# Performance work log

Measured on AMD Instinct MI355X. Metric: run time of the kernel, lower is better.

The kernel has to match this reference:

```python
import jax, jax.numpy as jnp
import numpy as np

L, H, NH, I = 6, 768, 12, 3072
DH = H // NH
EPS = 1e-12


def setup_inputs() -> dict:
    key = jax.random.key(0)
    ks = jax.random.split(key, 17)
    B, S = 16, 512
    s = lambda k, shape, fan: jax.random.normal(k, shape, jnp.float32) * (1.0 / np.sqrt(fan))
    return {
        "hidden_states": jax.random.normal(ks[0], (B, S, H), jnp.float32),
        "Wq": s(ks[1], (L, H, H), H), "bq": jnp.zeros((L, H), jnp.float32),
        "Wk": s(ks[2], (L, H, H), H), "bk": jnp.zeros((L, H), jnp.float32),
        "Wv": s(ks[3], (L, H, H), H), "bv": jnp.zeros((L, H), jnp.float32),
        "Wo": s(ks[4], (L, H, H), H), "bo": jnp.zeros((L, H), jnp.float32),
        "g1": jnp.ones((L, H), jnp.float32), "b1": jnp.zeros((L, H), jnp.float32),
        "Wi": s(ks[5], (L, H, I), H), "bi": jnp.zeros((L, I), jnp.float32),
        "Wo2": s(ks[6], (L, I, H), I), "bo2": jnp.zeros((L, H), jnp.float32),
        "g2": jnp.ones((L, H), jnp.float32), "b2": jnp.zeros((L, H), jnp.float32),
    }


def _layernorm(x, g, b):
    m = jnp.mean(x, axis=-1, keepdims=True)
    v = jnp.mean(jnp.square(x - m), axis=-1, keepdims=True)
    return (x - m) * jax.lax.rsqrt(v + EPS) * g + b


def _encoder(h, params):
    def layer_fn(h, p):
        Wq, bq, Wk, bk, Wv, bv, Wo, bo, g1, b1, Wi, bi, Wo2, bo2, g2, b2 = p
        B, S, _ = h.shape
        q = (h @ Wq + bq).reshape(B, S, NH, DH)
        k = (h @ Wk + bk).reshape(B, S, NH, DH)
        v = (h @ Wv + bv).reshape(B, S, NH, DH)
        scores = jnp.einsum("bshd,bthd->bhst", q, k) / np.sqrt(DH).astype(np.float32)
        probs = jax.nn.softmax(scores, axis=-1)  # dropout is identity in eval
        ctx = jnp.einsum("bhst,bthd->bshd", probs, v).reshape(B, S, H)
        attn_out = _layernorm(ctx @ Wo + bo + h, g1, b1)
        inter = jax.nn.gelu(attn_out @ Wi + bi, approximate=False)
        out = _layernorm(inter @ Wo2 + bo2 + attn_out, g2, b2)
        return out, None

    h, _ = jax.lax.scan(layer_fn, h, params)
    return h


def reference(hidden_states, Wq, bq, Wk, bk, Wv, bv, Wo, bo, g1, b1, Wi, bi, Wo2, bo2, g2, b2):
    params = (Wq, bq, Wk, bk, Wv, bv, Wo, bo, g1, b1, Wi, bi, Wo2, bo2, g2, b2)
    return _encoder(hidden_states, params)
```

## Files before the change

### kernel.cpp

```cpp
#include <hip/hip_runtime.h>
#include <hip/hip_bf16.h>
#include <math.h>

#define LNUM  6
#define HDIM  768
#define NHEAD 12
#define DHEAD 64
#define IDIM  3072
#define NB    16
#define SEQ   512
#define MTOK  (NB*SEQ)
#define NQKV  (3*HDIM)

typedef __bf16 bf16;
typedef __bf16 bf16x4 __attribute__((ext_vector_type(4)));
typedef __bf16 bf16x8 __attribute__((ext_vector_type(8)));
typedef float  f32x4  __attribute__((ext_vector_type(4)));

__device__ __forceinline__ void async_copy16(const bf16* g, bf16* l) {
  __builtin_amdgcn_global_load_lds((__attribute__((address_space(1))) void*)g,
                                   (__attribute__((address_space(3))) void*)l,
                                   16, 0, 0);
}

__device__ __forceinline__ float gelu_fast(float t) {
  const float u = 0.7978845608f * (t + 0.044715f * t * t * t);
  const float e = __expf(-2.f * fabsf(u));
  const float th = (1.f - e) / (1.f + e);
  return 0.5f * t * (1.f + copysignf(th, u));
}

__global__ void detect_k(const unsigned short* __restrict__ probe, int* __restrict__ flag)
{
  __shared__ int sc[4];
  const int tid = threadIdx.x;
  int cnt = 0;
#pragma unroll
  for (int j = 0; j < 16; j++) {
    const unsigned short w = probe[tid * 16 + j];
    const int e = (w >> 7) & 0xFF;
    cnt += (e >= 90 && e <= 130) ? 1 : 0;
  }
#pragma unroll
  for (int o = 32; o; o >>= 1) cnt += __shfl_xor(cnt, o);
  if ((tid & 63) == 0) sc[tid >> 6] = cnt;
  __syncthreads();
  if (tid == 0) flag[0] = ((sc[0] + sc[1] + sc[2] + sc[3]) < 3482) ? 1 : 0;
}

__global__ void cvt1d_k(const void* __restrict__ src, bf16* __restrict__ dst,
                        int n, const int* __restrict__ flag)
{
  const int i = blockIdx.x * 256 + threadIdx.x;
  if (i < n)
    dst[i] = (*flag) ? (bf16)((const float*)src)[i] : ((const bf16*)src)[i];
}

__global__ void cvt_slice_k(const void* __restrict__ src, bf16* __restrict__ dst,
                            int perL, int off, int dstStride, int total,
                            const int* __restrict__ flag)
{
  const int i = blockIdx.x * 256 + threadIdx.x;
  if (i < total) {
    const int l = i / perL, c = i - l * perL;
    const bf16 v = (*flag) ? (bf16)((const float*)src)[i] : ((const bf16*)src)[i];
    dst[l * dstStride + off + c] = v;
  }
}

__global__ void wtrans_k(const void* __restrict__ src, bf16* __restrict__ dst,
                         int K, int N, int layer, int dstLS, int dstOff,
                         const int* __restrict__ flag)
{
  __shared__ bf16 t[32][33];
  const size_t sOff = (size_t)(blockIdx.z + layer) * K * N;
  const size_t dOff = (size_t)blockIdx.z * dstLS + dstOff;
  const int n0 = blockIdx.x * 32, k0 = blockIdx.y * 32;
  const int tx = threadIdx.x, ty = threadIdx.y;
  const int f = *flag;
#pragma unroll
  for (int i = 0; i < 4; i++) {
    const size_t idx = sOff + (size_t)(k0 + ty*4 + i) * N + n0 + tx;
    t[ty*4+i][tx] = f ? (bf16)((const float*)src)[idx] : ((const bf16*)src)[idx];
  }
  __syncthreads();
#pragma unroll
  for (int i = 0; i < 4; i++)
    dst[dOff + (size_t)(n0 + ty*4 + i) * K + k0 + tx] = t[tx][ty*4+i];
}

#define STAGE2(DA, DB, KK) do {                                                \
    _Pragma("unroll")                                                          \
    for (int p = 0; p < BM/64; p++)                                            \
      async_copy16(gA + (size_t)p * 64 * sA + (KK),                            \
                   &DA[(wave*16)*32 + p*64*32]);                               \
    _Pragma("unroll")                                                          \
    for (int p = 0; p < BN/64; p++)                                            \
      async_copy16(gB + (size_t)p * 64 * sB + (KK),                            \
                   &DB[(wave*16)*32 + p*64*32]);                               \
  } while (0)

#define COMP2(SA, SB) do {                                                     \
    bf16x8 af[MT], bfv[NT];                                                    \
    _Pragma("unroll")                                                          \
    for (int i = 0; i < MT; i++)                                               \
      af[i] = *(const bf16x8*)&SA[(wm*(MT*16) + i*16 + l16) * 32               \
                                  + (quad ^ swz) * 8];                         \
    _Pragma("unroll")                                                          \
    for (int j = 0; j < NT; j++)                                               \
      bfv[j] = *(const bf16x8*)&SB[(wn*(NT*16) + j*16 + l16) * 32              \
                                   + (quad ^ swz) * 8];                        \
    _Pragma("unroll")                                                          \
    for (int i = 0; i < MT; i++)                                               \
      _Pragma("unroll")                                                        \
      for (int j = 0; j < NT; j++)                                             \
        acc[i][j] = __builtin_amdgcn_mfma_f32_16x16x32_bf16(                   \
            af[i], bfv[j], acc[i][j], 0, 0, 0);                                \
  } while (0)

template<int BM, int BN, int MT, int NT, int EPI, int XS>
__global__ __launch_bounds__(256)
void gemm_bt(const bf16* __restrict__ A, const bf16* __restrict__ Bt,
             float* __restrict__ Cf, bf16* __restrict__ Cb,
             bf16* __restrict__ Cb2, bf16* __restrict__ Cb3,
             const bf16* __restrict__ bias, const bf16* __restrict__ res,
             int K, int sA, int sB, int sC)
{
  __shared__ __align__(16) bf16 A0[BM*32];
  __shared__ __align__(16) bf16 B0[BN*32];
  __shared__ __align__(16) bf16 A1[BM*32];
  __shared__ __align__(16) bf16 B1[BN*32];
  const int tid  = threadIdx.x;
  const int wave = tid >> 6;
  const int lane = tid & 63;
  const int quad = lane >> 4;
  const int l16  = lane & 15;
  const int wm = wave >> 1, wn = wave & 1;
  const int swz = (l16 >> 1) & 3;

  int bx = blockIdx.x, by = blockIdx.y;
  if (XS) {
    if ((gridDim.y & 7) == 0) {
      const int id  = by * gridDim.x + bx;
      const int xcd = id & 7, slot = id >> 3;
      bx = slot % gridDim.x;
      by = (slot / gridDim.x) * 8 + xcd;
    }
  }
  const int m0 = by * BM;
  const int n0 = bx * BN;
  const int srow = tid >> 2;
  const int scol = (((tid & 3) ^ ((tid >> 3) & 3))) * 8;

  const bf16* gA = A + (size_t)(m0 + srow) * sA + scol;
  const bf16* gB = Bt + (size_t)(n0 + srow) * sB + scol;

  f32x4 acc[MT][NT];
  const f32x4 fzero = {0.f, 0.f, 0.f, 0.f};
#pragma unroll
  for (int i = 0; i < MT; i++)
#pragma unroll
    for (int j = 0; j < NT; j++) acc[i][j] = fzero;

  STAGE2(A0, B0, 0);
  __syncthreads();
  for (int k0 = 0; k0 < K; k0 += 64) {
    STAGE2(A1, B1, k0 + 32);
    COMP2(A0, B0);
    __syncthreads();
    if (k0 + 64 < K) STAGE2(A0, B0, k0 + 64);
    COMP2(A1, B1);
    __syncthreads();
  }

#pragma unroll
  for (int i = 0; i < MT; i++) {
    const int mtile = m0 + wm*(MT*16) + i*16 + quad*4;
#pragma unroll
    for (int j = 0; j < NT; j++) {
      const int nn = n0 + wn*(NT*16) + j*16 + l16;
      const float bv = bias ? (float)bias[nn] : 0.f;
      if (EPI == 5) {
        if (nn < HDIM) {
#pragma unroll
          for (int r = 0; r < 4; r++)
            Cb[(size_t)(mtile + r) * HDIM + nn] = (bf16)((acc[i][j][r] + bv) * 0.125f);
        } else if (nn < 2*HDIM) {
#pragma unroll
          for (int r = 0; r < 4; r++)
            Cb2[(size_t)(mtile + r) * HDIM + (nn - HDIM)] = (bf16)(acc[i][j][r] + bv);
        } else {
          const int nn2 = nn - 2*HDIM;
          const int bb = mtile >> 9, s = mtile & 511;
          const int hh = nn2 >> 6, dd = nn2 & 63;
          const size_t base = ((size_t)(bb*NHEAD + hh) * DHEAD + dd) * SEQ + s;
          bf16x4 pk;
#pragma unroll
          for (int r = 0; r < 4; r++) pk[r] = (bf16)(acc[i][j][r] + bv);
          *(bf16x4*)(Cb3 + base) = pk;
        }
      } else {
#pragma unroll
        for (int r = 0; r < 4; r++) {
          const int mm = mtile + r;
          const size_t idx = (size_t)mm * sC + nn;
          const float v = acc[i][j][r];
          if (EPI == 2) Cf[idx] = v + bv + (float)res[idx];
          else if (EPI == 3) Cb[idx] = (bf16)gelu_fast(v + bv);
        }
      }
    }
  }
}

__global__ __launch_bounds__(256)
void flash_k(const bf16* __restrict__ qb, const bf16* __restrict__ kb,
             const bf16* __restrict__ vt, bf16* __restrict__ ctxb)
{
  __shared__ __align__(16) bf16 Qs[128][72];
  __shared__ __align__(16) bf16 Ks[64][72];
  __shared__ __align__(16) bf16 Vs[64][72];
  __shared__ __align__(16) bf16 Ps[128][72];
  const int tid = threadIdx.x;
  const int wave = tid >> 6, lane = tid & 63;
  const int quad = lane >> 4, l16 = lane & 15;
  const int z = blockIdx.y;
  const int b = z / NHEAD, h = z - b * NHEAD;
  const int qt = blockIdx.x;
  const size_t qRow0 = (size_t)b * SEQ + qt * 128;

#pragma unroll
  for (int r = 0; r < 4; r++) {
    const int idx = tid + r * 256;
    const int row = idx >> 3, c8 = (idx & 7) * 8;
    *(bf16x8*)&Qs[row][c8] =
        *(const bf16x8*)&qb[(qRow0 + row) * HDIM + h * DHEAD + c8];
  }

  f32x4 Oacc[2][4];
  float mrow[2][4], lrow[2][4];
#pragma unroll
  for (int i = 0; i < 2; i++)
#pragma unroll
    for (int n = 0; n < 4; n++) Oacc[i][n] = (f32x4){0.f,0.f,0.f,0.f};
#pragma unroll
  for (int i = 0; i < 2; i++)
#pragma unroll
    for (int r = 0; r < 4; r++) { mrow[i][r] = -3.0e38f; lrow[i][r] = 0.f; }

  for (int j = 0; j < 8; j++) {
    __syncthreads();
#pragma unroll
    for (int r = 0; r < 2; r++) {
      const int idx = tid + r * 256;
      const int row = idx >> 3, c8 = (idx & 7) * 8;
      *(bf16x8*)&Ks[row][c8] =
          *(const bf16x8*)&kb[((size_t)b*SEQ + j*64 + row) * HDIM + h*DHEAD + c8];
      *(bf16x8*)&Vs[row][c8] =
          *(const bf16x8*)&vt[((size_t)z*DHEAD + row) * SEQ + j*64 + c8];
    }
    __syncthreads();

    f32x4 Sacc[2][4];
#pragma unroll
    for (int i = 0; i < 2; i++)
#pragma unroll
      for (int n = 0; n < 4; n++) Sacc[i][n] = (f32x4){0.f,0.f,0.f,0.f};
#pragma unroll
    for (int kk = 0; kk < 2; kk++) {
      bf16x8 af[2], bv[4];
#pragma unroll
      for (int i = 0; i < 2; i++)
        af[i] = *(const bf16x8*)&Qs[wave*32 + i*16 + l16][kk*32 + quad*8];
#pragma unroll
      for (int n = 0; n < 4; n++)
        bv[n] = *(const bf16x8*)&Ks[n*16 + l16][kk*32 + quad*8];
#pragma unroll
      for (int i = 0; i < 2; i++)
#pragma unroll
        for (int n = 0; n < 4; n++)
          Sacc[i][n] = __builtin_amdgcn_mfma_f32_16x16x32_bf16(af[i], bv[n], Sacc[i][n], 0,0,0);
    }

    float alpha[2][4];
#pragma unroll
    for (int i = 0; i < 2; i++)
#pragma unroll
      for (int r = 0; r < 4; r++) {
        float mx = Sacc[i][0][r];
#pragma unroll
        for (int n = 1; n < 4; n++) mx = fmaxf(mx, Sacc[i][n][r]);
#pragma unroll
        for (int o = 8; o; o >>= 1) mx = fmaxf(mx, __shfl_xor(mx, o));
        const float mn = fmaxf(mrow[i][r], mx);
        const float a = __expf(mrow[i][r] - mn);
        float rs = 0.f;
#pragma unroll
        for (int n = 0; n < 4; n++) {
          const float p = __expf(Sacc[i][n][r] - mn);
          Sacc[i][n][r] = p; rs += p;
        }
#pragma unroll
        for (int o = 8; o; o >>= 1) rs += __shfl_xor(rs, o);
        lrow[i][r] = lrow[i][r] * a + rs;
        mrow[i][r] = mn;
        alpha[i][r] = a;
      }

#pragma unroll
    for (int i = 0; i < 2; i++)
#pragma unroll
      for (int n = 0; n < 4; n++)
#pragma unroll
        for (int r = 0; r < 4; r++)
          Ps[wave*32 + i*16 + quad*4 + r][n*16 + l16] = (bf16)Sacc[i][n][r];
    __syncthreads();

#pragma unroll
    for (int i = 0; i < 2; i++)
#pragma unroll
      for (int n = 0; n < 4; n++)
#pragma unroll
        for (int r = 0; r < 4; r++) Oacc[i][n][r] *= alpha[i][r];
#pragma unroll
    for (int kk = 0; kk < 2; kk++) {
      bf16x8 af[2], bv[4];
#pragma unroll
      for (int i = 0; i < 2; i++)
        af[i] = *(const bf16x8*)&Ps[wave*32 + i*16 + l16][kk*32 + quad*8];
#pragma unroll
      for (int n = 0; n < 4; n++)
        bv[n] = *(const bf16x8*)&Vs[n*16 + l16][kk*32 + quad*8];
#pragma unroll
      for (int i = 0; i < 2; i++)
#pragma unroll
        for (int n = 0; n < 4; n++)
          Oacc[i][n] = __builtin_amdgcn_mfma_f32_16x16x32_bf16(af[i], bv[n], Oacc[i][n], 0,0,0);
    }
  }

#pragma unroll
  for (int i = 0; i < 2; i++)
#pragma unroll
    for (int r = 0; r < 4; r++) {
      const float inv = 1.f / lrow[i][r];
      const size_t tok = qRow0 + wave*32 + i*16 + quad*4 + r;
#pragma unroll
      for (int n = 0; n < 4; n++)
        ctxb[tok * HDIM + h*DHEAD + n*16 + l16] = (bf16)(Oacc[i][n][r] * inv);
    }
}

__global__ void layernorm_k(const float* __restrict__ x, const bf16* __restrict__ g,
                            const bf16* __restrict__ b, bf16* __restrict__ yb,
                            void* __restrict__ dout, int last, const int* __restrict__ flag)
{
  __shared__ float sred[4];
  const int row = blockIdx.x;
  const int tid = threadIdx.x;
  const float* xr = x + (size_t)row * HDIM;
  const float v0 = xr[tid], v1 = xr[tid+256], v2 = xr[tid+512];
  float s = v0 + v1 + v2;
#pragma unroll
  for (int o = 32; o; o >>= 1) s += __shfl_xor(s, o);
  if ((tid & 63) == 0) sred[tid >> 6] = s;
  __syncthreads();
  const float mean = (sred[0]+sred[1]+sred[2]+sred[3]) * (1.f/768.f);
  __syncthreads();
  const float d0 = v0-mean, d1 = v1-mean, d2 = v2-mean;
  float vs = d0*d0 + d1*d1 + d2*d2;
#pragma unroll
  for (int o = 32; o; o >>= 1) vs += __shfl_xor(vs, o);
  if ((tid & 63) == 0) sred[tid >> 6] = vs;
  __syncthreads();
  const float var = (sred[0]+sred[1]+sred[2]+sred[3]) * (1.f/768.f);
  const float rs  = rsqrtf(var + 1e-12f);
  const float y0 = d0*rs*(float)g[tid]     + (float)b[tid];
  const float y1 = d1*rs*(float)g[tid+256] + (float)b[tid+256];
  const float y2 = d2*rs*(float)g[tid+512] + (float)b[tid+512];
  bf16* ybr = yb + (size_t)row * HDIM;
  ybr[tid]     = (bf16)y0;
  ybr[tid+256] = (bf16)y1;
  ybr[tid+512] = (bf16)y2;
  if (last) {
    if (*flag) {
      float* o = (float*)dout + (size_t)row * HDIM;
      o[tid] = y0; o[tid+256] = y1; o[tid+512] = y2;
    } else {
      bf16* o = (bf16*)dout + (size_t)row * HDIM;
      o[tid] = (bf16)y0; o[tid+256] = (bf16)y1; o[tid+512] = (bf16)y2;
    }
  }
}

extern "C" void kernel_launch(void* const* d_in, const int* in_sizes, int n_in,
                              void* d_out, int out_size, void* d_ws, size_t ws_size,
                              hipStream_t stream)
{
  (void)in_sizes; (void)n_in; (void)out_size;

  char* ws = (char*)d_ws;
  size_t off = 0;
  auto carve = [&](size_t bytes) -> char* {
    char* p = ws + off; off += (bytes + 255) & ~(size_t)255; return p;
  };
  int*   flag = (int*)carve(256);
  bf16*  hcur = (bf16*)carve((size_t)MTOK*HDIM*2);
  bf16*  qb   = (bf16*)carve((size_t)MTOK*HDIM*2);
  bf16*  kb   = (bf16*)carve((size_t)MTOK*HDIM*2);
  bf16*  vt   = (bf16*)carve((size_t)MTOK*HDIM*2);
  bf16*  ctxb = (bf16*)carve((size_t)MTOK*HDIM*2);
  float* x1   = (float*)carve((size_t)MTOK*HDIM*4);
  bf16*  aob  = kb;

  bf16* nbqkv = (bf16*)carve((size_t)LNUM*NQKV*2);
  bf16* nbo   = (bf16*)carve((size_t)LNUM*HDIM*2);
  bf16* ng1   = (bf16*)carve((size_t)LNUM*HDIM*2);
  bf16* nb1   = (bf16*)carve((size_t)LNUM*HDIM*2);
  bf16* nbi   = (bf16*)carve((size_t)LNUM*IDIM*2);
  bf16* nbo2  = (bf16*)carve((size_t)LNUM*HDIM*2);
  bf16* ng2   = (bf16*)carve((size_t)LNUM*HDIM*2);
  bf16* nb2   = (bf16*)carve((size_t)LNUM*HDIM*2);

  const size_t wAllBytes = (size_t)LNUM*(NQKV*HDIM + HDIM*HDIM + 2*HDIM*IDIM)*2;
  const bool preAll = ws_size >= off + wAllBytes + (size_t)256*IDIM*2 + (1u<<20);
  bf16 *wqkvt=0, *wot=0, *wit=0, *wo2t=0, *bufA=0, *bufB=0;
  if (preAll) {
    wqkvt = (bf16*)carve((size_t)LNUM*NQKV*HDIM*2);
    wot   = (bf16*)carve((size_t)LNUM*HDIM*HDIM*2);
    wit   = (bf16*)carve((size_t)LNUM*HDIM*IDIM*2);
    wo2t  = (bf16*)carve((size_t)LNUM*HDIM*IDIM*2);
  } else {
    bufA = (bf16*)carve((size_t)HDIM*IDIM*2);
    bufB = (bf16*)carve((size_t)HDIM*IDIM*2);
  }

  const size_t unionAvail = (ws_size > off) ? (ws_size - off) : 0;
  int RM = 256;
  { const int rms[6] = {8192,4096,2048,1024,512,256};
    for (int i = 0; i < 6; i++)
      if ((size_t)rms[i]*IDIM*2 <= unionAvail) { RM = rms[i]; break; } }
  bf16* interb = (bf16*)(ws + off);

  detect_k<<<1, 256, 0, stream>>>((const unsigned short*)d_in[1], flag);
  cvt1d_k<<<(MTOK*HDIM+255)/256, 256, 0, stream>>>(d_in[0], hcur, MTOK*HDIM, flag);
  cvt_slice_k<<<(LNUM*HDIM+255)/256, 256, 0, stream>>>(d_in[2], nbqkv, HDIM, 0,      NQKV, LNUM*HDIM, flag);
  cvt_slice_k<<<(LNUM*HDIM+255)/256, 256, 0, stream>>>(d_in[4], nbqkv, HDIM, HDIM,   NQKV, LNUM*HDIM, flag);
  cvt_slice_k<<<(LNUM*HDIM+255)/256, 256, 0, stream>>>(d_in[6], nbqkv, HDIM, 2*HDIM, NQKV, LNUM*HDIM, flag);
  cvt1d_k<<<(LNUM*HDIM+255)/256, 256, 0, stream>>>(d_in[8],  nbo,  LNUM*HDIM, flag);
  cvt1d_k<<<(LNUM*HDIM+255)/256, 256, 0, stream>>>(d_in[9],  ng1,  LNUM*HDIM, flag);
  cvt1d_k<<<(LNUM*HDIM+255)/256, 256, 0, stream>>>(d_in[10], nb1,  LNUM*HDIM, flag);
  cvt1d_k<<<(LNUM*IDIM+255)/256, 256, 0, stream>>>(d_in[12], nbi,  LNUM*IDIM, flag);
  cvt1d_k<<<(LNUM*HDIM+255)/256, 256, 0, stream>>>(d_in[14], nbo2, LNUM*HDIM, flag);
  cvt1d_k<<<(LNUM*HDIM+255)/256, 256, 0, stream>>>(d_in[15], ng2,  LNUM*HDIM, flag);
  cvt1d_k<<<(LNUM*HDIM+255)/256, 256, 0, stream>>>(d_in[16], nb2,  LNUM*HDIM, flag);

  const dim3 tb(32, 8);
  if (preAll) {
    wtrans_k<<<dim3(HDIM/32, HDIM/32, LNUM), tb, 0, stream>>>(d_in[1], wqkvt, HDIM, HDIM, 0, NQKV*HDIM, 0,           flag);
    wtrans_k<<<dim3(HDIM/32, HDIM/32, LNUM), tb, 0, stream>>>(d_in[3], wqkvt, HDIM, HDIM, 0, NQKV*HDIM, HDIM*HDIM,   flag);
    wtrans_k<<<dim3(HDIM/32, HDIM/32, LNUM), tb, 0, stream>>>(d_in[5], wqkvt, HDIM, HDIM, 0, NQKV*HDIM, 2*HDIM*HDIM, flag);
    wtrans_k<<<dim3(HDIM/32, HDIM/32, LNUM), tb, 0, stream>>>(d_in[7], wot,  HDIM, HDIM, 0, HDIM*HDIM, 0, flag);
    wtrans_k<<<dim3(IDIM/32, HDIM/32, LNUM), tb, 0, stream>>>(d_in[11], wit,  HDIM, IDIM, 0, HDIM*IDIM, 0, flag);
    wtrans_k<<<dim3(HDIM/32, IDIM/32, LNUM), tb, 0, stream>>>(d_in[13], wo2t, IDIM, HDIM, 0, HDIM*IDIM, 0, flag);
  }

  for (int l = 0; l < LNUM; l++) {
    const bf16* hin = hcur;

    const bf16* WqkvT;
    if (preAll) WqkvT = wqkvt + (size_t)l * NQKV * HDIM;
    else {
      wtrans_k<<<dim3(HDIM/32, HDIM/32, 1), tb, 0, stream>>>(d_in[1], bufA, HDIM, HDIM, l, 0, 0,           flag);
      wtrans_k<<<dim3(HDIM/32, HDIM/32, 1), tb, 0, stream>>>(d_in[3], bufA, HDIM, HDIM, l, 0, HDIM*HDIM,   flag);
      wtrans_k<<<dim3(HDIM/32, HDIM/32, 1), tb, 0, stream>>>(d_in[5], bufA, HDIM, HDIM, l, 0, 2*HDIM*HDIM, flag);
      WqkvT = bufA;
    }
    gemm_bt<128,128,4,4,5,1><<<dim3(NQKV/128, MTOK/128), 256, 0, stream>>>(
        hin, WqkvT, nullptr, qb, kb, vt, nbqkv + (size_t)l*NQKV, nullptr,
        HDIM, HDIM, HDIM, HDIM);

    flash_k<<<dim3(SEQ/128, NB*NHEAD), 256, 0, stream>>>(qb, kb, vt, ctxb);

    const bf16* WoT;
    if (preAll) WoT = wot + (size_t)l * HDIM * HDIM;
    else {
      wtrans_k<<<dim3(HDIM/32, HDIM/32, 1), tb, 0, stream>>>(d_in[7], bufA, HDIM, HDIM, l, 0, 0, flag);
      WoT = bufA;
    }
    gemm_bt<128,128,4,4,2,1><<<dim3(HDIM/128, MTOK/128), 256, 0, stream>>>(
        ctxb, WoT, x1, nullptr, nullptr, nullptr, nbo + l*HDIM, hin,
        HDIM, HDIM, HDIM, HDIM);
    layernorm_k<<<MTOK, 256, 0, stream>>>(x1, ng1 + l*HDIM, nb1 + l*HDIM, aob,
                                          d_out, 0, flag);

    const bf16 *WiT, *Wo2T;
    if (preAll) { WiT = wit + (size_t)l*HDIM*IDIM; Wo2T = wo2t + (size_t)l*HDIM*IDIM; }
    else {
      wtrans_k<<<dim3(IDIM/32, HDIM/32, 1), tb, 0, stream>>>(d_in[11], bufA, HDIM, IDIM, l, 0, 0, flag);
      wtrans_k<<<dim3(HDIM/32, IDIM/32, 1), tb, 0, stream>>>(d_in[13], bufB, IDIM, HDIM, l, 0, 0, flag);
      WiT = bufA; Wo2T = bufB;
    }
    for (int r0 = 0; r0 < MTOK; r0 += RM) {
      gemm_bt<128,128,4,4,3,1><<<dim3(IDIM/128, RM/128), 256, 0, stream>>>(
          aob + (size_t)r0*HDIM, WiT, nullptr, interb, nullptr, nullptr,
          nbi + (size_t)l*IDIM, nullptr, HDIM, HDIM, HDIM, IDIM);
      gemm_bt<128,128,4,4,2,1><<<dim3(HDIM/128, RM/128), 256, 0, stream>>>(
          interb, Wo2T, x1 + (size_t)r0*HDIM, nullptr, nullptr, nullptr,
          nbo2 + l*HDIM, aob + (size_t)r0*HDIM, IDIM, IDIM, IDIM, HDIM);
    }
    layernorm_k<<<MTOK, 256, 0, stream>>>(x1, ng2 + l*HDIM, nb2 + l*HDIM, hcur,
                                          d_out, (l == LNUM-1) ? 1 : 0, flag);
  }
}
```

Before: 2.056 ms.

## Triple-buffer GEMM LDS stages with explicit vmcnt waits and raw barriers

Replaces the double-buffered K loop of the bf16 MFMA GEMM with a three-stage LDS ring. Each step issues the async global-to-LDS copy two tiles ahead, waits with s_waitcnt vmcnt(4) so only the newest stage stays in flight, then computes between raw s_barriers. Loads past the end of K are clamped to the last tile, so they become redundant copies rather than being skipped. The aim is to hide global load latency better, at the cost of more LDS per block, some extra loads at the tail, and a wait count that assumes a fixed number of copies per stage. A launch-bounds hint asking for 3 blocks per SIMD is also added.

```diff
diff --git a/kernel.cpp b/kernel.cpp
--- a/kernel.cpp
+++ b/kernel.cpp
@@ -89,18 +89,19 @@
     dst[dOff + (size_t)(n0 + ty*4 + i) * K + k0 + tx] = t[tx][ty*4+i];
 }
 
-#define STAGE2(DA, DB, KK) do {                                                \
+#define STAGE3(DA, DB, KK) do {                                                \
+    const int kk_ = ((KK) < K) ? (KK) : (K - 32);                              \
     _Pragma("unroll")                                                          \
     for (int p = 0; p < BM/64; p++)                                            \
-      async_copy16(gA + (size_t)p * 64 * sA + (KK),                            \
+      async_copy16(gA + (size_t)p * 64 * sA + kk_,                             \
                    &DA[(wave*16)*32 + p*64*32]);                               \
     _Pragma("unroll")                                                          \
     for (int p = 0; p < BN/64; p++)                                            \
-      async_copy16(gB + (size_t)p * 64 * sB + (KK),                            \
+      async_copy16(gB + (size_t)p * 64 * sB + kk_,                             \
                    &DB[(wave*16)*32 + p*64*32]);                               \
   } while (0)
 
-#define COMP2(SA, SB) do {                                                     \
+#define COMP3(SA, SB) do {                                                     \
     bf16x8 af[MT], bfv[NT];                                                    \
     _Pragma("unroll")                                                          \
     for (int i = 0; i < MT; i++)                                               \
@@ -118,8 +119,16 @@
             af[i], bfv[j], acc[i][j], 0, 0, 0);                                \
   } while (0)
 
+#define PIPE_STEP(SA, SB, DA, DB, KK) do {                                     \
+    STAGE3(DA, DB, KK);                                                        \
+    asm volatile("s_waitcnt vmcnt(4)" ::: "memory");                           \
+    __builtin_amdgcn_s_barrier();                                              \
+    COMP3(SA, SB);                                                             \
+    __builtin_amdgcn_s_barrier();                                              \
+  } while (0)
+
 template<int BM, int BN, int MT, int NT, int EPI, int XS>
-__global__ __launch_bounds__(256)
+__global__ __launch_bounds__(256, 3)
 void gemm_bt(const bf16* __restrict__ A, const bf16* __restrict__ Bt,
              float* __restrict__ Cf, bf16* __restrict__ Cb,
              bf16* __restrict__ Cb2, bf16* __restrict__ Cb3,
@@ -130,6 +139,8 @@
   __shared__ __align__(16) bf16 B0[BN*32];
   __shared__ __align__(16) bf16 A1[BM*32];
   __shared__ __align__(16) bf16 B1[BN*32];
+  __shared__ __align__(16) bf16 A2[BM*32];
+  __shared__ __align__(16) bf16 B2[BN*32];
   const int tid  = threadIdx.x;
   const int wave = tid >> 6;
   const int lane = tid & 63;
@@ -162,15 +173,12 @@
 #pragma unroll
     for (int j = 0; j < NT; j++) acc[i][j] = fzero;
 
-  STAGE2(A0, B0, 0);
-  __syncthreads();
-  for (int k0 = 0; k0 < K; k0 += 64) {
-    STAGE2(A1, B1, k0 + 32);
-    COMP2(A0, B0);
-    __syncthreads();
-    if (k0 + 64 < K) STAGE2(A0, B0, k0 + 64);
-    COMP2(A1, B1);
-    __syncthreads();
+  STAGE3(A0, B0, 0);
+  STAGE3(A1, B1, 32);
+  for (int k0 = 0; k0 < K; k0 += 96) {
+    PIPE_STEP(A0, B0, A2, B2, k0 + 64);
+    PIPE_STEP(A1, B1, A0, B0, k0 + 96);
+    PIPE_STEP(A2, B2, A1, B1, k0 + 128);
   }
 
 #pragma unroll
```

Result: faster. 1.864 ms (-9.4%).
